# Optimization experiments

Measured on AMD Instinct MI355X. Metric: run time of the kernel, lower is better.

The kernel has to match this reference:

```python
import jax, jax.numpy as jnp
import numpy as np

SIGMA_MIN = 0.01
BPTT = 6
GAMMA = 1.0
LOG2PI = float(np.log(2.0 * np.pi))


def setup_inputs() -> dict:
    key = jax.random.key(0)
    ks = jax.random.split(key, 12)
    T, B, MD, TD, H, E, S = 512, 128, 31, 2, 512, 256, 128

    def g(k, shape, s):
        return jax.random.normal(k, shape, dtype=jnp.float32) * s

    return dict(
        x=g(ks[0], (T, B, MD), 1.0),
        t=jax.random.uniform(ks[1], (T, B, TD), dtype=jnp.float32),
        mask=jnp.ones((T, B), dtype=jnp.float32),
        # embed_x: Linear(marker_dim -> 256) + ReLU
        W_embed=g(ks[2], (E, MD), 1.0 / np.sqrt(MD)),
        b_embed=jnp.zeros((E,), jnp.float32),
        # GRUCell(input=256, hidden=H): torch layout [3H, in], gate order r,z,n
        W_ih=g(ks[3], (3 * H, E), 1.0 / np.sqrt(H)),
        b_ih=jnp.zeros((3 * H,), jnp.float32),
        W_hh=g(ks[4], (3 * H, H), 1.0 / np.sqrt(H)),
        b_hh=jnp.zeros((3 * H,), jnp.float32),
        # embed_hidden_state: Linear(H -> 128) + ReLU
        W_he=g(ks[5], (S, H), 1.0 / np.sqrt(H)),
        b_he=jnp.zeros((S,), jnp.float32),
        # output_x_mu / output_x_logvar: Linear(128 -> marker_dim)
        W_mu=g(ks[6], (MD, S), 1.0 / np.sqrt(S)),
        b_mu=jnp.zeros((MD,), jnp.float32),
        W_lv=g(ks[7], (MD, S), 1.0 / np.sqrt(S)),
        b_lv=jnp.zeros((MD,), jnp.float32),
        # RMTPP intensity params: h_influence (Linear 128->1, no bias),
        # scalar time_influence and base_intensity parameters
        h_influence=g(ks[8], (S,), 0.01),
        time_influence=jnp.ones((1, 1, 1), jnp.float32),
        base_intensity=jnp.zeros((1, 1, 1), jnp.float32),
    )


def _model(x, t, mask, W_embed, b_embed, W_ih, b_ih, W_hh, b_hh,
           W_he, b_he, W_mu, b_mu, W_lv, b_lv,
           h_influence, time_influence, base_intensity):
    T, B, _ = x.shape
    H = W_hh.shape[1]

    # input embedding (ReLU MLP), then precompute all input-side gate GEMMs in one batched matmul
    phi = jax.nn.relu(jnp.einsum('tbm,em->tbe', x, W_embed) + b_embed)          # [T,B,256]
    x_gates = jnp.einsum('tbe,ge->tbg', phi, W_ih) + b_ih                       # [T,B,3H]

    # truncated-BPTT detach pattern: h is detached at steps where seq % bptt == 0
    detach = (jnp.arange(T) % BPTT) == 0

    def step(h, inp):
        xg, d = inp
        h = jnp.where(d, jax.lax.stop_gradient(h), h)  # value unchanged; grad cut
        hg = h @ W_hh.T + b_hh
        xr, xz, xn = jnp.split(xg, 3, axis=-1)
        hr, hz, hn = jnp.split(hg, 3, axis=-1)
        r = jax.nn.sigmoid(xr + hr)
        z = jax.nn.sigmoid(xz + hz)
        n = jnp.tanh(xn + r * hn)
        h_new = (1.0 - z) * n + z * h
        return h_new, h  # collect pre-update state => h_0..h_{T-1} == h[:-1]

    h0 = jnp.zeros((B, H), jnp.float32)
    _, hs = jax.lax.scan(step, h0, (x_gates, detach))                           # [T,B,H]

    he = jax.nn.relu(jnp.einsum('tbh,sh->tbs', hs, W_he) + b_he)               # [T,B,128]

    # marker (real) Gaussian log-likelihood with sigma clamped at sigma_min
    mu = jnp.einsum('tbs,ms->tbm', he, W_mu) + b_mu
    logvar = jnp.einsum('tbs,ms->tbm', he, W_lv) + b_lv
    sigma = jnp.maximum(jnp.exp(0.5 * logvar), SIGMA_MIN)
    marker_ll = jnp.sum(-0.5 * jnp.square((x - mu) / sigma) - jnp.log(sigma)
                        - 0.5 * LOG2PI, axis=-1)                                # [T,B]

    # RMTPP point-process log-likelihood of the time gap d = t[:,:,1]
    ti = time_influence.reshape(())
    bi = base_intensity.reshape(())
    past = jnp.einsum('tbs,s->tb', he, h_influence)                             # [T,B]
    term1 = past + ti * t[:, :, 1] + bi
    time_ll = term1 + (jnp.exp(past + bi) - jnp.exp(term1)) / ti                # [T,B]

    marker_loss = jnp.sum((-marker_ll * mask)[1:])
    time_loss = jnp.sum((-time_ll * mask)[1:])
    return GAMMA * time_loss + marker_loss


def reference(x, t, mask, W_embed, b_embed, W_ih, b_ih, W_hh, b_hh,
              W_he, b_he, W_mu, b_mu, W_lv, b_lv,
              h_influence, time_influence, base_intensity):
    return _model(x, t, mask, W_embed, b_embed, W_ih, b_ih, W_hh, b_hh,
                  W_he, b_he, W_mu, b_mu, W_lv, b_lv,
                  h_influence, time_influence, base_intensity)
```

## Files before the change

### kernel.cpp

```cpp
#include <hip/hip_runtime.h>
#include <cstddef>
#include <cstdint>

#define T_LEN 512
#define B_SZ  128
#define MD    31
#define E_SZ  256
#define H_SZ  512
#define S_SZ  128
#define GAMMA_F 1.0f
#define LOG001   -4.605170185988091f
#define HALF_L2PI 0.9189385332046727f

typedef __attribute__((ext_vector_type(8))) short bf16x8;
typedef __attribute__((ext_vector_type(4))) float f32x4;

#define ACT_PITCH 536
#define PHI_PITCH 264
#define GP        36
#define HS_PITCH  516
#define WM_PITCH  132
#define CNT_STRIDE 16

#define SMEM_BYTES 58240
#define R_ACT  0
#define R_PHI  17152
#define R_GS   34048
#define L_HST  0
#define L_HES  33024
#define L_WMU  41280
#define L_WLV  49464
#define L_HINF 57648

__device__ inline unsigned short f2bf(float f) {
    union { float f; unsigned u; } v; v.f = f;
    unsigned r = v.u + 0x7FFFu + ((v.u >> 16) & 1u);
    return (unsigned short)(r >> 16);
}
__device__ inline float bf2f(unsigned short u) {
    union { unsigned u; float f; } v; v.u = (unsigned)u << 16; return v.f;
}
__device__ inline unsigned long long llc_load_u64(const unsigned long long* p) {
    return __hip_atomic_load(p, __ATOMIC_RELAXED, __HIP_MEMORY_SCOPE_AGENT);
}
__device__ inline unsigned llc_load_u32(const unsigned* p) {
    return __hip_atomic_load(p, __ATOMIC_RELAXED, __HIP_MEMORY_SCOPE_AGENT);
}

__global__ __launch_bounds__(256) void prep(
    const float* __restrict__ x, const float* __restrict__ W_embed,
    const float* __restrict__ b_embed,
    const float* __restrict__ W_ih, const float* __restrict__ W_hh,
    unsigned short* __restrict__ wpack, unsigned short* __restrict__ phi,
    unsigned* __restrict__ hx, unsigned* __restrict__ cnt, float* __restrict__ out) {
    const int blk = blockIdx.x;
    if (blk < 512) {
        const int n = 1536 * 768;
        for (int i = blk * 256 + threadIdx.x; i < n; i += 512 * 256) {
            int col = i / 768, k = i - col * 768;
            float v = (k < H_SZ) ? W_hh[col * H_SZ + k] : W_ih[col * E_SZ + (k - H_SZ)];
            wpack[i] = f2bf(v);
        }
        if (blk < 64) {
            #pragma unroll
            for (int k = 0; k < 4; ++k) hx[blk * 1024 + k * 256 + threadIdx.x] = 0u;
        }
        if (blk == 0) {
            for (int k = threadIdx.x; k < 128 * CNT_STRIDE; k += 256) cnt[k] = 0u;
            if (threadIdx.x == 0) out[0] = 0.f;
        }
    } else {
        __shared__ float xs[8][32];
        const int e = threadIdx.x;
        float w[MD];
        #pragma unroll
        for (int m = 0; m < MD; ++m) w[m] = W_embed[e * MD + m];
        const float be = b_embed[e];
        const int nblocks = (T_LEN * B_SZ) / 8;
        for (int rb = blk - 512; rb < nblocks; rb += 1024) {
            const int r0 = rb * 8;
            if (threadIdx.x < 8 * MD)
                xs[threadIdx.x / MD][threadIdx.x % MD] = x[(size_t)r0 * MD + threadIdx.x];
            __syncthreads();
            #pragma unroll
            for (int i = 0; i < 8; ++i) {
                float acc = be;
                #pragma unroll
                for (int m = 0; m < MD; ++m) acc = fmaf(xs[i][m], w[m], acc);
                phi[(size_t)(r0 + i) * E_SZ + e] = f2bf(fmaxf(acc, 0.f));
            }
            __syncthreads();
        }
    }
}

__global__ __launch_bounds__(384) void fused_persist(
    const unsigned short* __restrict__ wpack, const unsigned short* __restrict__ phi,
    unsigned* __restrict__ hx, float* __restrict__ hs,
    const float* __restrict__ b_ih, const float* __restrict__ b_hh,
    unsigned* __restrict__ cnt,
    const float* __restrict__ W_he, const float* __restrict__ b_he,
    const float* __restrict__ W_mu, const float* __restrict__ b_mu,
    const float* __restrict__ W_lv, const float* __restrict__ b_lv,
    const float* __restrict__ h_inf, const float* __restrict__ time_inf,
    const float* __restrict__ base_int, const float* __restrict__ x,
    const float* __restrict__ t_in, const float* __restrict__ mask,
    float* __restrict__ out) {
    __shared__ __align__(16) char smem[SMEM_BYTES];
    const int tid = threadIdx.x;

    if (blockIdx.x < 128) {
        short* act_s = (short*)(smem + R_ACT);
        short* phi_s0 = (short*)(smem + R_PHI);
        short* phi_s1 = (short*)(smem + R_PHI) + 16 * PHI_PITCH;
        float* g_s = (float*)(smem + R_GS);

        const int bt = blockIdx.x & 7, ct = blockIdx.x >> 3;
        const int b0 = bt * 16, j0 = ct * 32;
        const int wid = tid >> 6, L = tid & 63;
        const int gt = wid >> 1, ch = wid & 1;
        const int n_loc = L & 15, kb2 = L >> 4;
        const int a_row = L & 15;

        const unsigned short* __restrict__ wrow =
            wpack + (size_t)(gt * 512 + j0 + ch * 16 + n_loc) * 768;
        bf16x8 Bf[24];
        #pragma unroll
        for (int i = 0; i < 24; ++i) Bf[i] = *(const bf16x8*)(wrow + i * 32 + kb2 * 8);

        const int g_row = tid >> 5, g_col = tid & 31;
        float bias_r = 0.f, bias_z = 0.f, bias_xn = 0.f, bias_hn = 0.f;
        if (tid < 256) {
            const int j = j0 + g_col;
            bias_r  = b_ih[j] + b_hh[j];
            bias_z  = b_ih[512 + j] + b_hh[512 + j];
            bias_xn = b_ih[1024 + j];
            bias_hn = b_hh[1024 + j];
        }
        float hold1 = 0.f, hold2 = 0.f;

        #pragma unroll
        for (int it = 0; it < 3; ++it) {
            const int c = tid + it * 384;
            if (c < 1024) {
                const int m = c >> 6, q = c & 63;
                *(unsigned long long*)(phi_s0 + m * PHI_PITCH + q * 4) =
                    *(const unsigned long long*)(phi + ((size_t)(b0 + m)) * E_SZ + q * 4);
            }
        }
        __syncthreads();

        for (int t = 0; t < T_LEN - 1; ++t) {
            const int buf = t & 1;
            const short* phi_cur = buf ? phi_s1 : phi_s0;
            const unsigned tg = (unsigned)t & 0xFFFFu;

            f32x4 accP = {0.f, 0.f, 0.f, 0.f};
            {
                const short* prow = phi_cur + a_row * PHI_PITCH;
                #pragma unroll
                for (int i = 16; i < 24; ++i) {
                    bf16x8 a = *(const bf16x8*)(prow + (i - 16) * 32 + kb2 * 8);
                    accP = __builtin_amdgcn_mfma_f32_16x16x32_bf16(a, Bf[i], accP, 0, 0, 0);
                }
            }

            const unsigned long long* hx64 =
                (const unsigned long long*)hx + ((size_t)(buf * 8 + bt)) * 4096;
            unsigned long long v[11];
            #pragma unroll
            for (int it = 0; it < 11; ++it) {
                const int c = tid + it * 384;
                if (c < 4096) v[it] = llc_load_u64(hx64 + c);
            }
            while (true) {
                unsigned bad = 0;
                #pragma unroll
                for (int it = 0; it < 11; ++it) {
                    const int c = tid + it * 384;
                    if (c < 4096) {
                        const unsigned t0 = (unsigned)v[it] & 0xFFFFu;
                        const unsigned t1 = (unsigned)(v[it] >> 32) & 0xFFFFu;
                        if ((t0 ^ tg) | (t1 ^ tg)) bad |= (1u << it);
                    }
                }
                if (bad == 0) break;
                __builtin_amdgcn_s_sleep(1);
                #pragma unroll
                for (int it = 0; it < 11; ++it)
                    if (bad & (1u << it)) v[it] = llc_load_u64(hx64 + tid + it * 384);
            }
            #pragma unroll
            for (int it = 0; it < 11; ++it) {
                const int c = tid + it * 384;
                if (c < 4096) {
                    const int ctp = c >> 8, w = c & 255, row = w >> 4, colp = w & 15;
                    const unsigned lo = (unsigned)(v[it] >> 16) & 0xFFFFu;
                    const unsigned hi = (unsigned)(v[it] >> 48) & 0xFFFFu;
                    *(unsigned*)(act_s + row * ACT_PITCH + ctp * 32 + colp * 2) = lo | (hi << 16);
                }
            }
            __syncthreads();
            if (tid == 0 && t)
                __hip_atomic_store(cnt + blockIdx.x * CNT_STRIDE, (unsigned)t,
                                   __ATOMIC_RELAXED, __HIP_MEMORY_SCOPE_AGENT);

            unsigned long long pv[3];
            const int tn = t + 1;
            if (tn < T_LEN - 1) {
                #pragma unroll
                for (int it = 0; it < 3; ++it) {
                    const int c = tid + it * 384;
                    if (c < 1024) {
                        const int m = c >> 6, q = c & 63;
                        pv[it] = *(const unsigned long long*)(
                            phi + ((size_t)tn * B_SZ + b0 + m) * E_SZ + q * 4);
                    }
                }
            }

            {
                const short* arow = act_s + a_row * ACT_PITCH;
                f32x4 acc0 = {0.f, 0.f, 0.f, 0.f};
                f32x4 acc1 = {0.f, 0.f, 0.f, 0.f};
                #pragma unroll
                for (int i = 0; i < 16; i += 2) {
                    bf16x8 a0 = *(const bf16x8*)(arow + i * 32 + kb2 * 8);
                    bf16x8 a1 = *(const bf16x8*)(arow + (i + 1) * 32 + kb2 * 8);
                    acc0 = __builtin_amdgcn_mfma_f32_16x16x32_bf16(a0, Bf[i], acc0, 0, 0, 0);
                    acc1 = __builtin_amdgcn_mfma_f32_16x16x32_bf16(a1, Bf[i + 1], acc1, 0, 0, 0);
                }
                if (gt < 2) {
                    #pragma unroll
                    for (int i2 = 0; i2 < 4; ++i2)
                        g_s[gt * 16 * GP + ((L >> 4) * 4 + i2) * GP + ch * 16 + n_loc] =
                            acc0[i2] + acc1[i2] + accP[i2];
                } else {
                    #pragma unroll
                    for (int i2 = 0; i2 < 4; ++i2) {
                        const int idx = ((L >> 4) * 4 + i2) * GP + ch * 16 + n_loc;
                        g_s[2 * 16 * GP + idx] = acc0[i2] + acc1[i2];
                        g_s[3 * 16 * GP + idx] = accP[i2];
                    }
                }
            }

            if (tn < T_LEN - 1) {
                short* pbuf = (tn & 1) ? phi_s1 : phi_s0;
                #pragma unroll
                for (int it = 0; it < 3; ++it) {
                    const int c = tid + it * 384;
                    if (c < 1024) {
                        const int m = c >> 6, q = c & 63;
                        *(unsigned long long*)(pbuf + m * PHI_PITCH + q * 4) = pv[it];
                    }
                }
            }
            __syncthreads();

            if (tid < 256) {
                const int nb = (t + 1) & 1;
                unsigned* hxdst = hx + ((size_t)(nb * 8 + bt) * 16 + ct) * 512;
                #pragma unroll
                for (int half = 0; half < 2; ++half) {
                    const int row = g_row + half * 8;
                    const int idx = row * GP + g_col;
                    float& hold = half ? hold2 : hold1;
                    const float pre_r = g_s[0 * 16 * GP + idx] + bias_r;
                    const float pre_z = g_s[1 * 16 * GP + idx] + bias_z;
                    const float hn    = g_s[2 * 16 * GP + idx] + bias_hn;
                    const float xn    = g_s[3 * 16 * GP + idx] + bias_xn;
                    const float r = 1.f / (1.f + __expf(-pre_r));
                    const float z = 1.f / (1.f + __expf(-pre_z));
                    const float e2 = __expf(-2.f * fmaf(r, hn, xn));
                    const float n = (1.f - e2) / (1.f + e2);
                    const float hnew = fmaf(z, hold - n, n);
                    hold = hnew;
                    __hip_atomic_store(
                        hs + (size_t)(t + 1) * B_SZ * H_SZ + (size_t)(b0 + row) * H_SZ + j0 + g_col,
                        hnew, __ATOMIC_RELAXED, __HIP_MEMORY_SCOPE_AGENT);
                    if (t < T_LEN - 2)
                        __hip_atomic_store(hxdst + row * 32 + g_col,
                                           ((unsigned)f2bf(hnew) << 16) | ((unsigned)(t + 1) & 0xFFFFu),
                                           __ATOMIC_RELAXED, __HIP_MEMORY_SCOPE_AGENT);
                }
            }
        }
        __syncthreads();
        if (tid == 0)
            __hip_atomic_store(cnt + blockIdx.x * CNT_STRIDE, (unsigned)(T_LEN - 1),
                               __ATOMIC_RELAXED, __HIP_MEMORY_SCOPE_AGENT);
    } else {
        float* hsT  = (float*)(smem + L_HST);
        float* he_s = (float*)(smem + L_HES);
        unsigned short* wmu_s = (unsigned short*)(smem + L_WMU);
        unsigned short* wlv_s = (unsigned short*)(smem + L_WLV);
        float* hinf_s = (float*)(smem + L_HINF);
        float* red    = (float*)(smem + L_HINF) + 128;

        const int i = blockIdx.x - 128;
        const int lb = i & 7, ls = i >> 3;
        const int b0 = lb * 16;

        for (int k = tid; k < MD * S_SZ; k += 384) {
            wmu_s[(k >> 7) * WM_PITCH + (k & 127)] = f2bf(W_mu[k]);
            wlv_s[(k >> 7) * WM_PITCH + (k & 127)] = f2bf(W_lv[k]);
        }
        if (tid < S_SZ) hinf_s[tid] = h_inf[tid];
        __syncthreads();

        float lacc = 0.f;
        for (int s = 0; s < 32; ++s) {
            const int t = 1 + ls + 16 * s;
            if (t > T_LEN - 1) break;
            if (tid < 64) {
                while (true) {
                    unsigned cv = 0xFFFFFFFFu;
                    if (tid < 16) cv = llc_load_u32(cnt + (lb + 8 * tid) * CNT_STRIDE);
                    if (__ballot(cv >= (unsigned)t) == ~0ull) break;
                    __builtin_amdgcn_s_sleep(64);
                }
            }
            __syncthreads();
            const unsigned long long* hs64 =
                (const unsigned long long*)(hs + ((size_t)t * B_SZ + b0) * H_SZ);
            #pragma unroll
            for (int it = 0; it < 11; ++it) {
                const int c = tid + it * 384;
                if (c < 4096) {
                    const int m = c >> 8, q = c & 255;
                    unsigned long long v = llc_load_u64(hs64 + (size_t)m * 256 + q);
                    *(unsigned long long*)(hsT + m * HS_PITCH + q * 2) = v;
                }
            }
            __syncthreads();
            if (tid < 256) {
                const int c = tid & 127, rg = tid >> 7;
                const float* __restrict__ wr = W_he + (size_t)c * H_SZ;
                float acc[8];
                #pragma unroll
                for (int ii = 0; ii < 8; ++ii) acc[ii] = b_he[c];
                for (int k = 0; k < H_SZ; k += 4) {
                    const float4 w4 = *(const float4*)(wr + k);
                    #pragma unroll
                    for (int ii = 0; ii < 8; ++ii) {
                        const float4 h4 = *(const float4*)(hsT + (rg * 8 + ii) * HS_PITCH + k);
                        acc[ii] = fmaf(w4.x, h4.x, acc[ii]);
                        acc[ii] = fmaf(w4.y, h4.y, acc[ii]);
                        acc[ii] = fmaf(w4.z, h4.z, acc[ii]);
                        acc[ii] = fmaf(w4.w, h4.w, acc[ii]);
                    }
                }
                #pragma unroll
                for (int ii = 0; ii < 8; ++ii)
                    he_s[(rg * 8 + ii) * 129 + c] = fmaxf(acc[ii], 0.f);
            }
            __syncthreads();
            if (tid < 256) {
                const int r = tid >> 4, q = tid & 15;
                const int row = t * B_SZ + b0 + r;
                const float mk = mask[row];
                #pragma unroll
                for (int pass = 0; pass < 2; ++pass) {
                    const int m = q + pass * 16;
                    if (m < MD) {
                        float mu = b_mu[m], lv = b_lv[m];
                        for (int c2 = 0; c2 < S_SZ; ++c2) {
                            const float h = he_s[r * 129 + c2];
                            mu = fmaf(h, bf2f(wmu_s[m * WM_PITCH + c2]), mu);
                            lv = fmaf(h, bf2f(wlv_s[m * WM_PITCH + c2]), lv);
                        }
                        const float lsg   = fmaxf(0.5f * lv, LOG001);
                        const float inv_s = __expf(-lsg);
                        const float zz    = (x[(size_t)row * MD + m] - mu) * inv_s;
                        lacc += (0.5f * zz * zz + lsg + HALF_L2PI) * mk;
                    }
                }
                if (q == 0) {
                    float past = 0.f;
                    for (int c2 = 0; c2 < S_SZ; ++c2)
                        past = fmaf(he_s[r * 129 + c2], hinf_s[c2], past);
                    const float ti = time_inf[0], bi = base_int[0];
                    const float dt = t_in[(size_t)row * 2 + 1];
                    const float term1 = past + ti * dt + bi;
                    const float tll = term1 + (__expf(past + bi) - __expf(term1)) / ti;
                    lacc += GAMMA_F * (-tll) * mk;
                }
            }
            __syncthreads();
        }
        #pragma unroll
        for (int off = 32; off > 0; off >>= 1) lacc += __shfl_down(lacc, off, 64);
        if ((tid & 63) == 0) red[tid >> 6] = lacc;
        __syncthreads();
        if (tid == 0) {
            float sum = 0.f;
            #pragma unroll
            for (int w = 0; w < 6; ++w) sum += red[w];
            atomicAdd(out, sum);
        }
    }
}

extern "C" void kernel_launch(void* const* d_in, const int* in_sizes, int n_in,
                              void* d_out, int out_size, void* d_ws, size_t ws_size,
                              hipStream_t stream) {
    const float* x       = (const float*)d_in[0];
    const float* t_in    = (const float*)d_in[1];
    const float* mask    = (const float*)d_in[2];
    const float* W_embed = (const float*)d_in[3];
    const float* b_embed = (const float*)d_in[4];
    const float* W_ih    = (const float*)d_in[5];
    const float* b_ih    = (const float*)d_in[6];
    const float* W_hh    = (const float*)d_in[7];
    const float* b_hh    = (const float*)d_in[8];
    const float* W_he    = (const float*)d_in[9];
    const float* b_he    = (const float*)d_in[10];
    const float* W_mu    = (const float*)d_in[11];
    const float* b_mu    = (const float*)d_in[12];
    const float* W_lv    = (const float*)d_in[13];
    const float* b_lv    = (const float*)d_in[14];
    const float* h_inf   = (const float*)d_in[15];
    const float* tinf    = (const float*)d_in[16];
    const float* bint    = (const float*)d_in[17];
    float* out = (float*)d_out;

    char* ws = (char*)d_ws;
    const size_t OFF_PHI = 0;
    const size_t OFF_HS  = 33554432ull;
    const size_t OFF_WP  = 167772160ull;
    const size_t OFF_HX  = 170131456ull;
    const size_t OFF_CNT = 170655744ull;
    const size_t TOTAL   = 170663936ull;
    if (ws_size < TOTAL) return;
    unsigned short* phi   = (unsigned short*)(ws + OFF_PHI);
    float*          hsbuf = (float*)(ws + OFF_HS);
    unsigned short* wpack = (unsigned short*)(ws + OFF_WP);
    unsigned*       hx    = (unsigned*)(ws + OFF_HX);
    unsigned*       cnt   = (unsigned*)(ws + OFF_CNT);

    prep<<<dim3(1536), 256, 0, stream>>>(x, W_embed, b_embed, W_ih, W_hh,
                                         wpack, phi, hx, cnt, out);

    void* args[] = {(void*)&wpack, (void*)&phi, (void*)&hx, (void*)&hsbuf,
                    (void*)&b_ih, (void*)&b_hh, (void*)&cnt,
                    (void*)&W_he, (void*)&b_he, (void*)&W_mu, (void*)&b_mu,
                    (void*)&W_lv, (void*)&b_lv, (void*)&h_inf, (void*)&tinf,
                    (void*)&bint, (void*)&x, (void*)&t_in, (void*)&mask, (void*)&out};
    hipLaunchCooperativeKernel((void*)fused_persist, dim3(256), dim3(384), args, 0, stream);
}
```

Before: 1.634 ms.

## Split hidden-state polling into two halves overlapped with recurrent MFMA

The per-step poll of the shared hidden-state buffer is split into two halves. All loads are issued before the phi MFMAs. The first half is validated, staged into shared memory and used for the first half of the recurrent MFMA before the second half is checked. This lets the block start computing while slower producers finish, and hides load latency behind the phi GEMM. It adds an extra __syncthreads per step and more live registers.

```diff
diff --git a/kernel.cpp b/kernel.cpp
--- a/kernel.cpp
+++ b/kernel.cpp
@@ -154,6 +154,20 @@
             const int buf = t & 1;
             const short* phi_cur = buf ? phi_s1 : phi_s0;
             const unsigned tg = (unsigned)t & 0xFFFFu;
+            const unsigned long long* hx64 =
+                (const unsigned long long*)hx + ((size_t)(buf * 8 + bt)) * 4096;
+
+            unsigned long long v1[6], v2[6];
+            #pragma unroll
+            for (int it = 0; it < 6; ++it) {
+                const int c = tid + it * 384;
+                if (c < 2048) v1[it] = llc_load_u64(hx64 + c);
+            }
+            #pragma unroll
+            for (int it = 0; it < 6; ++it) {
+                const int c = 2048 + tid + it * 384;
+                if (c < 4096) v2[it] = llc_load_u64(hx64 + c);
+            }
 
             f32x4 accP = {0.f, 0.f, 0.f, 0.f};
             {
@@ -165,38 +179,30 @@
                 }
             }
 
-            const unsigned long long* hx64 =
-                (const unsigned long long*)hx + ((size_t)(buf * 8 + bt)) * 4096;
-            unsigned long long v[11];
-            #pragma unroll
-            for (int it = 0; it < 11; ++it) {
-                const int c = tid + it * 384;
-                if (c < 4096) v[it] = llc_load_u64(hx64 + c);
-            }
             while (true) {
                 unsigned bad = 0;
                 #pragma unroll
-                for (int it = 0; it < 11; ++it) {
+                for (int it = 0; it < 6; ++it) {
                     const int c = tid + it * 384;
-                    if (c < 4096) {
-                        const unsigned t0 = (unsigned)v[it] & 0xFFFFu;
-                        const unsigned t1 = (unsigned)(v[it] >> 32) & 0xFFFFu;
+                    if (c < 2048) {
+                        const unsigned t0 = (unsigned)v1[it] & 0xFFFFu;
+                        const unsigned t1 = (unsigned)(v1[it] >> 32) & 0xFFFFu;
                         if ((t0 ^ tg) | (t1 ^ tg)) bad |= (1u << it);
                     }
                 }
                 if (bad == 0) break;
                 __builtin_amdgcn_s_sleep(1);
                 #pragma unroll
-                for (int it = 0; it < 11; ++it)
-                    if (bad & (1u << it)) v[it] = llc_load_u64(hx64 + tid + it * 384);
-            }
-            #pragma unroll
-            for (int it = 0; it < 11; ++it) {
+                for (int it = 0; it < 6; ++it)
+                    if (bad & (1u << it)) v1[it] = llc_load_u64(hx64 + tid + it * 384);
+            }
+            #pragma unroll
+            for (int it = 0; it < 6; ++it) {
                 const int c = tid + it * 384;
-                if (c < 4096) {
+                if (c < 2048) {
                     const int ctp = c >> 8, w = c & 255, row = w >> 4, colp = w & 15;
-                    const unsigned lo = (unsigned)(v[it] >> 16) & 0xFFFFu;
-                    const unsigned hi = (unsigned)(v[it] >> 48) & 0xFFFFu;
+                    const unsigned lo = (unsigned)(v1[it] >> 16) & 0xFFFFu;
+                    const unsigned hi = (unsigned)(v1[it] >> 48) & 0xFFFFu;
                     *(unsigned*)(act_s + row * ACT_PITCH + ctp * 32 + colp * 2) = lo | (hi << 16);
                 }
             }
@@ -219,12 +225,52 @@
                 }
             }
 
+            f32x4 acc0 = {0.f, 0.f, 0.f, 0.f};
+            f32x4 acc1 = {0.f, 0.f, 0.f, 0.f};
             {
                 const short* arow = act_s + a_row * ACT_PITCH;
-                f32x4 acc0 = {0.f, 0.f, 0.f, 0.f};
-                f32x4 acc1 = {0.f, 0.f, 0.f, 0.f};
-                #pragma unroll
-                for (int i = 0; i < 16; i += 2) {
+                #pragma unroll
+                for (int i = 0; i < 8; i += 2) {
+                    bf16x8 a0 = *(const bf16x8*)(arow + i * 32 + kb2 * 8);
+                    bf16x8 a1 = *(const bf16x8*)(arow + (i + 1) * 32 + kb2 * 8);
+                    acc0 = __builtin_amdgcn_mfma_f32_16x16x32_bf16(a0, Bf[i], acc0, 0, 0, 0);
+                    acc1 = __builtin_amdgcn_mfma_f32_16x16x32_bf16(a1, Bf[i + 1], acc1, 0, 0, 0);
+                }
+            }
+
+            while (true) {
+                unsigned bad = 0;
+                #pragma unroll
+                for (int it = 0; it < 6; ++it) {
+                    const int c = 2048 + tid + it * 384;
+                    if (c < 4096) {
+                        const unsigned t0 = (unsigned)v2[it] & 0xFFFFu;
+                        const unsigned t1 = (unsigned)(v2[it] >> 32) & 0xFFFFu;
+                        if ((t0 ^ tg) | (t1 ^ tg)) bad |= (1u << it);
+                    }
+                }
+                if (bad == 0) break;
+                __builtin_amdgcn_s_sleep(1);
+                #pragma unroll
+                for (int it = 0; it < 6; ++it)
+                    if (bad & (1u << it)) v2[it] = llc_load_u64(hx64 + 2048 + tid + it * 384);
+            }
+            #pragma unroll
+            for (int it = 0; it < 6; ++it) {
+                const int c = 2048 + tid + it * 384;
+                if (c < 4096) {
+                    const int ctp = c >> 8, w = c & 255, row = w >> 4, colp = w & 15;
+                    const unsigned lo = (unsigned)(v2[it] >> 16) & 0xFFFFu;
+                    const unsigned hi = (unsigned)(v2[it] >> 48) & 0xFFFFu;
+                    *(unsigned*)(act_s + row * ACT_PITCH + ctp * 32 + colp * 2) = lo | (hi << 16);
+                }
+            }
+            __syncthreads();
+
+            {
+                const short* arow = act_s + a_row * ACT_PITCH;
+                #pragma unroll
+                for (int i = 8; i < 16; i += 2) {
                     bf16x8 a0 = *(const bf16x8*)(arow + i * 32 + kb2 * 8);
                     bf16x8 a1 = *(const bf16x8*)(arow + (i + 1) * 32 + kb2 * 8);
                     acc0 = __builtin_amdgcn_mfma_f32_16x16x32_bf16(a0, Bf[i], acc0, 0, 0, 0);
```

After: 2.083 ms. +27.5%, slower.
